# Kernel optimization log

Hardware: AMD Instinct MI355X
Metric: run time of the kernel (lower is better)

## Reference

```python
import jax, jax.numpy as jnp
import numpy as np

N = 100000; E = 3200000; B = 4096
F = 128; H = 128; T1 = 574; T2 = 152; MH = 128
BN_INV = float(1.0 / np.sqrt(1.0 + 1e-5))  # eval-mode BatchNorm1d, running_mean=0, running_var=1


def setup_inputs() -> dict:
    key = jax.random.key(0)
    ks = jax.random.split(key, 16)
    def w(k, shape):
        return (jax.random.normal(k, shape, jnp.float32) / np.sqrt(shape[0])).astype(jnp.float32)
    return {
        "feats": jax.random.normal(ks[0], (N, F), jnp.float32),
        "src": jax.random.randint(ks[1], (E,), 0, N, dtype=jnp.int32),
        "dst": jax.random.randint(ks[2], (E,), 0, N, dtype=jnp.int32),
        "graph_ids": jnp.sort(jax.random.randint(ks[3], (N,), 0, B, dtype=jnp.int32)),
        "W1": w(ks[4], (F, H)), "b1": jnp.zeros((H,), jnp.float32),
        "resW1": w(ks[5], (F, H)), "resb1": jnp.zeros((H,), jnp.float32),
        "W2": w(ks[6], (H, H)), "b2": jnp.zeros((H,), jnp.float32),
        "resW2": w(ks[7], (H, H)), "resb2": jnp.zeros((H,), jnp.float32),
        "aw_W": w(ks[8], (H, 1)), "aw_b": jnp.zeros((1,), jnp.float32),
        "orW1": w(ks[9], (2 * H, MH)), "orb1": jnp.zeros((MH,), jnp.float32),
        "org": jnp.ones((MH,), jnp.float32), "orbeta": jnp.zeros((MH,), jnp.float32),
        "orW2": w(ks[10], (MH, T1)), "orb2": jnp.zeros((T1,), jnp.float32),
        "scW1": w(ks[11], (2 * H + T1, MH)), "scb1": jnp.zeros((MH,), jnp.float32),
        "scg": jnp.ones((MH,), jnp.float32), "scbeta": jnp.zeros((MH,), jnp.float32),
        "scW2": w(ks[12], (MH, T2)), "scb2": jnp.zeros((T2,), jnp.float32),
    }


def _gcn_layer(feats, src, dst, W, b, resW, resb, out_norm, in_norm):
    # GraphConv with norm='both': D_out^{-1/2} on source, sum over edges, D_in^{-1/2} on dest.
    h = (feats * out_norm[:, None]) @ W                       # [N, H]
    agg = jax.ops.segment_sum(h[src], dst, num_segments=N)    # gather-compute-scatter
    out = jax.nn.relu(agg * in_norm[:, None] + b)             # activation inside GraphConv
    return out + jax.nn.relu(feats @ resW + resb)             # dgllife residual branch


def _mlp(x, Wa, ba, gam, bet, Wb, bb):
    # dgllife MLPPredictor: Dropout(0) -> Linear -> ReLU -> BatchNorm1d(eval) -> Linear
    z = jax.nn.relu(x @ Wa + ba)
    z = gam * (z * BN_INV) + bet
    return z @ Wb + bb


def _forward(feats, src, dst, graph_ids, W1, b1, resW1, resb1, W2, b2, resW2, resb2,
             aw_W, aw_b, orW1, orb1, org, orbeta, orW2, orb2,
             scW1, scb1, scg, scbeta, scW2, scb2):
    ones = jnp.ones((E,), jnp.float32)
    out_norm = jnp.clip(jax.ops.segment_sum(ones, src, num_segments=N), 1.0) ** -0.5
    in_norm = jnp.clip(jax.ops.segment_sum(ones, dst, num_segments=N), 1.0) ** -0.5
    h = _gcn_layer(feats, src, dst, W1, b1, resW1, resb1, out_norm, in_norm)
    h = _gcn_layer(h, src, dst, W2, b2, resW2, resb2, out_norm, in_norm)
    # WeightedSumAndMax readout
    aw = jax.nn.sigmoid(h @ aw_W + aw_b)                      # [N, 1] atom weights
    hsum = jax.ops.segment_sum(aw * h, graph_ids, num_segments=B)
    hmax = jax.ops.segment_max(h, graph_ids, num_segments=B)
    hmax = jnp.where(jnp.isfinite(hmax), hmax, 0.0)           # guard empty graphs
    g = jnp.concatenate([hsum, hmax], axis=1)                 # [B, 2H]
    or_logits = _mlp(g, orW1, orb1, org, orbeta, orW2, orb2)  # [B, T1]
    scent = _mlp(jnp.concatenate([g, or_logits], axis=1), scW1, scb1, scg, scbeta, scW2, scb2)
    return or_logits, scent


def reference(feats, src, dst, graph_ids, W1, b1, resW1, resb1, W2, b2, resW2, resb2,
              aw_W, aw_b, orW1, orb1, org, orbeta, orW2, orb2,
              scW1, scb1, scg, scbeta, scW2, scb2):
    return _forward(feats, src, dst, graph_ids, W1, b1, resW1, resb1, W2, b2, resW2, resb2,
                    aw_W, aw_b, orW1, orb1, org, orbeta, orW2, orb2,
                    scW1, scb1, scg, scbeta, scW2, scb2)
```

## Files before the change

### kernel.cpp

```cpp
#include <hip/hip_runtime.h>

#define NN 100000
#define EE 3200000
#define NGRAPH 4096
#define BN_INV_F 0.99999500003749981f
#define PAD 80
#define SHIFT 8
#define NBUCK 391
#define CHUNK 8192
#define NBLK 391
#define SCAN_N (2 * NBUCK * NBLK)
#define SCHUNK 2048
#define SBLKS ((SCAN_N + SCHUNK - 1) / SCHUNK)

typedef __attribute__((ext_vector_type(8))) short short8v;
typedef __attribute__((ext_vector_type(4))) float f32x4;

__device__ inline ushort f2bf(float f) {
  uint u = __builtin_bit_cast(uint, f);
  u += 0x7fff + ((u >> 16) & 1);
  return (ushort)(u >> 16);
}
__device__ inline float bf_lo(uint v) { return __builtin_bit_cast(float, v << 16); }
__device__ inline float bf_hi(uint v) { return __builtin_bit_cast(float, v & 0xffff0000u); }

__global__ __launch_bounds__(256) void count_ab(const int* __restrict__ src,
                                                const int* __restrict__ dst,
                                                int* __restrict__ cnt) {
  __shared__ int hd[NBUCK], hs[NBUCK];
  int t = threadIdx.x, blk = blockIdx.x;
  for (int i = t; i < NBUCK; i += 256) { hd[i] = 0; hs[i] = 0; }
  __syncthreads();
  int base = blk * CHUNK;
#pragma unroll 4
  for (int j = 0; j < 32; j++) {
    int e = base + j * 256 + t;
    if (e < EE) {
      atomicAdd(&hd[((unsigned)dst[e]) >> SHIFT], 1);
      atomicAdd(&hs[((unsigned)src[e]) >> SHIFT], 1);
    }
  }
  __syncthreads();
  for (int i = t; i < NBUCK; i += 256) {
    cnt[i * NBLK + blk] = hd[i];
    cnt[(NBUCK + i) * NBLK + blk] = hs[i];
  }
}

__global__ __launch_bounds__(256) void scan1(const int* __restrict__ cnt,
                                             int* __restrict__ partial) {
  __shared__ int red[256];
  int b = blockIdx.x, t = threadIdx.x;
  int s = 0;
  for (int j = 0; j < 8; j++) { int i = b * SCHUNK + j * 256 + t; if (i < SCAN_N) s += cnt[i]; }
  red[t] = s;
  __syncthreads();
  for (int off = 128; off > 0; off >>= 1) {
    if (t < off) red[t] += red[t + off];
    __syncthreads();
  }
  if (t == 0) partial[b] = red[0];
}

__global__ void scan2(int* __restrict__ partial) {
  if (threadIdx.x == 0) {
    int run = 0;
    for (int i = 0; i < SBLKS; i++) { int v = partial[i]; partial[i] = run; run += v; }
  }
}

__global__ __launch_bounds__(256) void scan3(int* __restrict__ cnt,
                                             const int* __restrict__ partial) {
  __shared__ int wsum[4];
  int b = blockIdx.x, t = threadIdx.x;
  int lane = t & 63, wid = t >> 6;
  int base = b * SCHUNK + t * 8;
  int v[8];
#pragma unroll
  for (int j = 0; j < 8; j++) { int i = base + j; v[j] = (i < SCAN_N) ? cnt[i] : 0; }
  int s = ((v[0] + v[1]) + (v[2] + v[3])) + ((v[4] + v[5]) + (v[6] + v[7]));
  int inc = s;
#pragma unroll
  for (int off = 1; off < 64; off <<= 1) {
    int u = __shfl_up(inc, off);
    if (lane >= off) inc += u;
  }
  if (lane == 63) wsum[wid] = inc;
  __syncthreads();
  int woff = 0;
  for (int w = 0; w < wid; w++) woff += wsum[w];
  int excl = partial[b] + woff + (inc - s);
#pragma unroll
  for (int j = 0; j < 8; j++) {
    int i = base + j;
    if (i < SCAN_N) cnt[i] = excl;
    excl += v[j];
  }
}

__global__ __launch_bounds__(256) void scatter_c(const int* __restrict__ src,
                                                 const int* __restrict__ dst,
                                                 const int* __restrict__ off,
                                                 int2* __restrict__ ebuf,
                                                 int* __restrict__ sbuf) {
  __shared__ int cd[NBUCK], cs[NBUCK];
  int t = threadIdx.x, blk = blockIdx.x;
  for (int i = t; i < NBUCK; i += 256) {
    cd[i] = off[i * NBLK + blk];
    cs[i] = off[(NBUCK + i) * NBLK + blk] - EE;
  }
  __syncthreads();
  int base = blk * CHUNK;
#pragma unroll 4
  for (int j = 0; j < 32; j++) {
    int e = base + j * 256 + t;
    if (e < EE) {
      int d = dst[e], s = src[e];
      int p = atomicAdd(&cd[((unsigned)d) >> SHIFT], 1);
      ebuf[p] = make_int2(d, s);
      int q = atomicAdd(&cs[((unsigned)s) >> SHIFT], 1);
      sbuf[q] = s;
    }
  }
}

__global__ __launch_bounds__(256) void pass_dd(const int* __restrict__ off,
                                               const int2* __restrict__ ebuf,
                                               const int* __restrict__ sbuf,
                                               int* __restrict__ csrp,
                                               int* __restrict__ icnt,
                                               float* __restrict__ inrm,
                                               float* __restrict__ onrm) {
  __shared__ int cur[256], cur2[256];
  int t = threadIdx.x, b = blockIdx.x;
  cur[t] = 0; cur2[t] = 0;
  __syncthreads();
  int node0 = b << SHIFT;
  int start = off[b * NBLK];
  int end = (b == NBUCK - 1) ? EE : off[(b + 1) * NBLK];
  for (int e = start + t; e < end; e += 256) {
    int2 p = ebuf[e];
    int pos = atomicAdd(&cur[p.x - node0], 1);
    if (pos < PAD) csrp[(size_t)p.x * PAD + pos] = p.y;
  }
  int s2 = off[(NBUCK + b) * NBLK] - EE;
  int e2 = (b == NBUCK - 1) ? EE : off[(NBUCK + b + 1) * NBLK] - EE;
  for (int e = s2 + t; e < e2; e += 256)
    atomicAdd(&cur2[sbuf[e] - node0], 1);
  __syncthreads();
  int node = node0 + t;
  if (node < NN) {
    int c = cur[t];
    icnt[node] = c;
    inrm[node] = rsqrtf(fmaxf((float)c, 1.f));
    onrm[node] = rsqrtf(fmaxf((float)cur2[t], 1.f));
  }
}

__global__ __launch_bounds__(256) void conv_all(
    const float* __restrict__ W1, const float* __restrict__ rW1,
    const float* __restrict__ W2, const float* __restrict__ rW2,
    const float* __restrict__ oW1, const float* __restrict__ oW2,
    const float* __restrict__ sW1, const float* __restrict__ sW2,
    ushort* __restrict__ Wt1, ushort* __restrict__ Wr1,
    ushort* __restrict__ Wt2, ushort* __restrict__ Wr2,
    ushort* __restrict__ Wm1, ushort* __restrict__ Wm2,
    ushort* __restrict__ Wm3, ushort* __restrict__ Wm4)
{
  int b = blockIdx.x;
  const float* W; ushort* O; int K, N, Kpad, c;
  if (b < 512) {
    int which = b >> 7; c = b & 127;
    K = 128; N = 128; Kpad = 128;
    W = which == 0 ? W1 : which == 1 ? rW1 : which == 2 ? W2 : rW2;
    O = which == 0 ? Wt1 : which == 1 ? Wr1 : which == 2 ? Wt2 : Wr2;
  } else if (b < 640)  { c = b - 512;  W = oW1; O = Wm1; K = 256; N = 128; Kpad = 256; }
  else if (b < 1216)   { c = b - 640;  W = oW2; O = Wm2; K = 128; N = 574; Kpad = 128; }
  else if (b < 1344)   { c = b - 1216; W = sW1; O = Wm3; K = 830; N = 128; Kpad = 832; }
  else                 { c = b - 1344; W = sW2; O = Wm4; K = 128; N = 152; Kpad = 128; }
  for (int k = threadIdx.x; k < Kpad; k += 256)
    O[(size_t)c * Kpad + k] = (c < N && k < K) ? f2bf(W[(size_t)k * N + c]) : (ushort)0;
}

__global__ __launch_bounds__(256) void conv_x(const float* __restrict__ X,
                                              ushort* __restrict__ Xb) {
  int i = blockIdx.x * 256 + threadIdx.x;
  float4 v = *(const float4*)&X[(size_t)i * 4];
  ushort o[4] = {f2bf(v.x), f2bf(v.y), f2bf(v.z), f2bf(v.w)};
  *(ushort4*)&Xb[(size_t)i * 4] = *(ushort4*)o;
}

__global__ __launch_bounds__(256) void gather_sc(const ushort* __restrict__ Xg,
                                                 const float* __restrict__ gscale,
                                                 const int* __restrict__ csrp,
                                                 const int* __restrict__ icnt,
                                                 ushort* __restrict__ Gbo) {
  int n  = blockIdx.x * 4 + (threadIdx.x >> 6);
  int c2 = threadIdx.x & 63;
  if (n >= NN) return;
  int cnt = icnt[n]; if (cnt > PAD) cnt = PAD;
  const int* row = csrp + (size_t)n * PAD;
  const uint* T32 = (const uint*)Xg;
  float a0 = 0.f, a1 = 0.f, b0 = 0.f, b1 = 0.f;
  float c0 = 0.f, c1 = 0.f, d0 = 0.f, d1 = 0.f;
  float e0 = 0.f, e1 = 0.f, f0 = 0.f, f1 = 0.f;
  float g0 = 0.f, g1 = 0.f, h0 = 0.f, h1 = 0.f;
  int j = 0;
  for (; j + 7 < cnt; j += 8) {
    int r0i = row[j],     r1i = row[j + 1], r2i = row[j + 2], r3i = row[j + 3];
    int r4i = row[j + 4], r5i = row[j + 5], r6i = row[j + 6], r7i = row[j + 7];
    float w0 = gscale[r0i], w1 = gscale[r1i], w2 = gscale[r2i], w3 = gscale[r3i];
    float w4 = gscale[r4i], w5 = gscale[r5i], w6 = gscale[r6i], w7 = gscale[r7i];
    uint v0 = T32[(size_t)r0i * 64 + c2];
    uint v1 = T32[(size_t)r1i * 64 + c2];
    uint v2 = T32[(size_t)r2i * 64 + c2];
    uint v3 = T32[(size_t)r3i * 64 + c2];
    uint v4 = T32[(size_t)r4i * 64 + c2];
    uint v5 = T32[(size_t)r5i * 64 + c2];
    uint v6 = T32[(size_t)r6i * 64 + c2];
    uint v7 = T32[(size_t)r7i * 64 + c2];
    a0 = fmaf(w0, bf_lo(v0), a0); a1 = fmaf(w0, bf_hi(v0), a1);
    b0 = fmaf(w1, bf_lo(v1), b0); b1 = fmaf(w1, bf_hi(v1), b1);
    c0 = fmaf(w2, bf_lo(v2), c0); c1 = fmaf(w2, bf_hi(v2), c1);
    d0 = fmaf(w3, bf_lo(v3), d0); d1 = fmaf(w3, bf_hi(v3), d1);
    e0 = fmaf(w4, bf_lo(v4), e0); e1 = fmaf(w4, bf_hi(v4), e1);
    f0 = fmaf(w5, bf_lo(v5), f0); f1 = fmaf(w5, bf_hi(v5), f1);
    g0 = fmaf(w6, bf_lo(v6), g0); g1 = fmaf(w6, bf_hi(v6), g1);
    h0 = fmaf(w7, bf_lo(v7), h0); h1 = fmaf(w7, bf_hi(v7), h1);
  }
  for (; j < cnt; j++) {
    int ri = row[j];
    float w = gscale[ri];
    uint v = T32[(size_t)ri * 64 + c2];
    a0 = fmaf(w, bf_lo(v), a0); a1 = fmaf(w, bf_hi(v), a1);
  }
  float s0 = ((a0 + b0) + (c0 + d0)) + ((e0 + f0) + (g0 + h0));
  float s1 = ((a1 + b1) + (c1 + d1)) + ((e1 + f1) + (g1 + h1));
  uint o = (uint)f2bf(s0) | ((uint)f2bf(s1) << 16);
  ((uint*)Gbo)[(size_t)n * 64 + c2] = o;
}

template<int MODE>
__global__ __launch_bounds__(256) void dual_gemm(
    const ushort* __restrict__ Gb, const ushort* __restrict__ Xr,
    const ushort* __restrict__ Wt, const ushort* __restrict__ Wr,
    const float* __restrict__ innorm,
    const float* __restrict__ bias, const float* __restrict__ resb,
    ushort* __restrict__ outb, float* __restrict__ outf,
    const float* __restrict__ awW, const float* __restrict__ awb,
    float* __restrict__ aw)
{
  int lane = threadIdx.x & 63;
  int wid  = threadIdx.x >> 6;
  int r0   = blockIdx.x * 64 + wid * 16;
  int cl = lane & 15, kh = lane >> 4;

  int arow = r0 + cl; if (arow > NN - 1) arow = NN - 1;
  short8v a1v[4], a2v[4];
#pragma unroll
  for (int kk = 0; kk < 4; kk++) {
    a1v[kk] = *(const short8v*)(Gb + (size_t)arow * 128 + kk * 32 + kh * 8);
    a2v[kk] = *(const short8v*)(Xr + (size_t)arow * 128 + kk * 32 + kh * 8);
  }

  f32x4 acc1[8], acc2[8];
#pragma unroll
  for (int i = 0; i < 8; i++) { acc1[i] = (f32x4){0.f,0.f,0.f,0.f}; acc2[i] = acc1[i]; }
#pragma unroll
  for (int ct = 0; ct < 8; ct++) {
#pragma unroll
    for (int kk = 0; kk < 4; kk++) {
      short8v bt = *(const short8v*)(Wt + (size_t)(ct * 16 + cl) * 128 + kk * 32 + kh * 8);
      short8v br = *(const short8v*)(Wr + (size_t)(ct * 16 + cl) * 128 + kk * 32 + kh * 8);
      acc1[ct] = __builtin_amdgcn_mfma_f32_16x16x32_bf16(a1v[kk], bt, acc1[ct], 0, 0, 0);
      acc2[ct] = __builtin_amdgcn_mfma_f32_16x16x32_bf16(a2v[kk], br, acc2[ct], 0, 0, 0);
    }
  }

#pragma unroll
  for (int r = 0; r < 4; r++) {
    int row = r0 + kh * 4 + r;
    if (row >= NN) continue;
    float inr = innorm[row];
    float pr = 0.f;
#pragma unroll
    for (int ct = 0; ct < 8; ct++) {
      int col = ct * 16 + cl;
      float g  = acc1[ct][r] * inr + bias[col];
      float rs = acc2[ct][r] + resb[col];
      float v = fmaxf(g, 0.f) + fmaxf(rs, 0.f);
      if (MODE == 1) outb[(size_t)row * 128 + col] = f2bf(v);
      else { outf[(size_t)row * 128 + col] = v; pr += v * awW[col]; }
    }
    if (MODE == 2) {
#pragma unroll
      for (int off = 1; off < 16; off <<= 1) pr += __shfl_xor(pr, off);
      if (cl == 0) aw[row] = 1.f / (1.f + expf(-(pr + awb[0])));
    }
  }
}

__global__ void readout_kernel(const float* __restrict__ h,
                               const float* __restrict__ aw,
                               const int* __restrict__ gid,
                               ushort* __restrict__ xc)
{
  int gg = blockIdx.x;
  int c  = threadIdx.x;
  int lo = 0, hi = NN;
  while (lo < hi) { int mid = (lo + hi) >> 1; if (gid[mid] < gg) lo = mid + 1; else hi = mid; }
  int start = lo;
  hi = NN;
  while (lo < hi) { int mid = (lo + hi) >> 1; if (gid[mid] < gg + 1) lo = mid + 1; else hi = mid; }
  int end = lo;
  float s = 0.f, m = 0.f;
  for (int n = start; n < end; n++) {
    float v = h[(size_t)n * 128 + c];
    s += aw[n] * v;
    m = fmaxf(m, v);
  }
  xc[(size_t)gg * 256 + c]       = f2bf(s);
  xc[(size_t)gg * 256 + 128 + c] = f2bf(m);
}

__global__ __launch_bounds__(256) void head2_mfma(
    const ushort* __restrict__ xc,
    const ushort* __restrict__ Wm1, const float* __restrict__ orb1,
    const float* __restrict__ org, const float* __restrict__ orbeta,
    const ushort* __restrict__ Wm2, const float* __restrict__ orb2,
    const ushort* __restrict__ Wm3, const float* __restrict__ scb1,
    const float* __restrict__ scg, const float* __restrict__ scbeta,
    const ushort* __restrict__ Wm4, const float* __restrict__ scb2,
    float* __restrict__ out_or, float* __restrict__ out_sc)
{
  __shared__ ushort zl[16][136];
  __shared__ ushort lg[16][584];
  int lane = threadIdx.x & 63;
  int wid  = threadIdx.x >> 6;
  int r0   = blockIdx.x * 16;
  int cl = lane & 15, kh = lane >> 4;
  int arow = r0 + cl;

  {
    short8v a[8];
#pragma unroll
    for (int kk = 0; kk < 8; kk++)
      a[kk] = *(const short8v*)(xc + (size_t)arow * 256 + kk * 32 + kh * 8);
    for (int ct = wid; ct < 8; ct += 4) {
      f32x4 acc = (f32x4){0.f, 0.f, 0.f, 0.f};
#pragma unroll
      for (int kk = 0; kk < 8; kk++) {
        short8v b = *(const short8v*)(Wm1 + (size_t)(ct * 16 + cl) * 256 + kk * 32 + kh * 8);
        acc = __builtin_amdgcn_mfma_f32_16x16x32_bf16(a[kk], b, acc, 0, 0, 0);
      }
      int col = ct * 16 + cl;
      float bz = orb1[col], gm = org[col], bt = orbeta[col];
#pragma unroll
      for (int r = 0; r < 4; r++) {
        float v = acc[r] + bz;
        zl[kh * 4 + r][col] = f2bf(gm * (fmaxf(v, 0.f) * BN_INV_F) + bt);
      }
    }
  }
  __syncthreads();

  {
    short8v za[4];
#pragma unroll
    for (int kk = 0; kk < 4; kk++)
      za[kk] = *(const short8v*)&zl[cl][kk * 32 + kh * 8];
    for (int ct = wid; ct < 36; ct += 4) {
      f32x4 acc = (f32x4){0.f, 0.f, 0.f, 0.f};
#pragma unroll
      for (int kk = 0; kk < 4; kk++) {
        short8v b = *(const short8v*)(Wm2 + (size_t)(ct * 16 + cl) * 128 + kk * 32 + kh * 8);
        acc = __builtin_amdgcn_mfma_f32_16x16x32_bf16(za[kk], b, acc, 0, 0, 0);
      }
      int col = ct * 16 + cl;
      if (col < 574) {
        float bz = orb2[col];
#pragma unroll
        for (int r = 0; r < 4; r++) {
          int row = r0 + kh * 4 + r;
          float v = acc[r] + bz;
          out_or[(size_t)row * 574 + col] = v;
          lg[kh * 4 + r][col] = f2bf(v);
        }
      } else {
#pragma unroll
        for (int r = 0; r < 4; r++) lg[kh * 4 + r][col] = 0;
      }
    }
  }
  __syncthreads();

  {
    short8v a[26];
#pragma unroll
    for (int kk = 0; kk < 8; kk++)
      a[kk] = *(const short8v*)(xc + (size_t)arow * 256 + kk * 32 + kh * 8);
#pragma unroll
    for (int kk = 8; kk < 26; kk++)
      a[kk] = *(const short8v*)&lg[cl][(kk - 8) * 32 + kh * 8];
    for (int ct = wid; ct < 8; ct += 4) {
      f32x4 acc = (f32x4){0.f, 0.f, 0.f, 0.f};
#pragma unroll
      for (int kk = 0; kk < 26; kk++) {
        short8v b = *(const short8v*)(Wm3 + (size_t)(ct * 16 + cl) * 832 + kk * 32 + kh * 8);
        acc = __builtin_amdgcn_mfma_f32_16x16x32_bf16(a[kk], b, acc, 0, 0, 0);
      }
      int col = ct * 16 + cl;
      float bz = scb1[col], gm = scg[col], bt = scbeta[col];
#pragma unroll
      for (int r = 0; r < 4; r++) {
        float v = acc[r] + bz;
        zl[kh * 4 + r][col] = f2bf(gm * (fmaxf(v, 0.f) * BN_INV_F) + bt);
      }
    }
  }
  __syncthreads();

  {
    short8v za[4];
#pragma unroll
    for (int kk = 0; kk < 4; kk++)
      za[kk] = *(const short8v*)&zl[cl][kk * 32 + kh * 8];
    for (int ct = wid; ct < 10; ct += 4) {
      f32x4 acc = (f32x4){0.f, 0.f, 0.f, 0.f};
#pragma unroll
      for (int kk = 0; kk < 4; kk++) {
        short8v b = *(const short8v*)(Wm4 + (size_t)(ct * 16 + cl) * 128 + kk * 32 + kh * 8);
        acc = __builtin_amdgcn_mfma_f32_16x16x32_bf16(za[kk], b, acc, 0, 0, 0);
      }
      int col = ct * 16 + cl;
      if (col < 152) {
        float bz = scb2[col];
#pragma unroll
        for (int r = 0; r < 4; r++) {
          int row = r0 + kh * 4 + r;
          out_sc[(size_t)row * 152 + col] = acc[r] + bz;
        }
      }
    }
  }
}

extern "C" void kernel_launch(void* const* d_in, const int* in_sizes, int n_in,
                              void* d_out, int out_size, void* d_ws, size_t ws_size,
                              hipStream_t stream) {
  const float* feats  = (const float*)d_in[0];
  const int*   src    = (const int*)d_in[1];
  const int*   dst    = (const int*)d_in[2];
  const int*   gid    = (const int*)d_in[3];
  const float* W1     = (const float*)d_in[4];
  const float* b1     = (const float*)d_in[5];
  const float* resW1  = (const float*)d_in[6];
  const float* resb1  = (const float*)d_in[7];
  const float* W2     = (const float*)d_in[8];
  const float* b2     = (const float*)d_in[9];
  const float* resW2  = (const float*)d_in[10];
  const float* resb2  = (const float*)d_in[11];
  const float* awW    = (const float*)d_in[12];
  const float* awb    = (const float*)d_in[13];
  const float* orW1   = (const float*)d_in[14];
  const float* orb1   = (const float*)d_in[15];
  const float* org    = (const float*)d_in[16];
  const float* orbeta = (const float*)d_in[17];
  const float* orW2   = (const float*)d_in[18];
  const float* orb2   = (const float*)d_in[19];
  const float* scW1   = (const float*)d_in[20];
  const float* scb1   = (const float*)d_in[21];
  const float* scg    = (const float*)d_in[22];
  const float* scbeta = (const float*)d_in[23];
  const float* scW2   = (const float*)d_in[24];
  const float* scb2   = (const float*)d_in[25];

  char* base = (char*)d_ws;
  ushort* Xb = (ushort*)base;
  ushort* Lb = Xb + (size_t)NN * 128;
  ushort* Gb = Lb + (size_t)NN * 128;
  float*  Hf = (float*)(Gb + (size_t)NN * 128);
  int2*   ebuf = (int2*)Hf;
  int*    sbuf = (int*)(Hf + (size_t)NN * 64);
  ushort* xc  = (ushort*)(Hf + (size_t)NN * 128);
  ushort* Wt1 = xc + (size_t)NGRAPH * 256;
  ushort* Wr1 = Wt1 + 128 * 128;
  ushort* Wt2 = Wr1 + 128 * 128;
  ushort* Wr2 = Wt2 + 128 * 128;
  ushort* Wm1 = Wr2 + 128 * 128;
  ushort* Wm2 = Wm1 + 128 * 256;
  ushort* Wm3 = Wm2 + 576 * 128;
  ushort* Wm4 = Wm3 + 128 * 832;
  float* onrm = (float*)(Wm4 + 160 * 128);
  float* inrm = onrm + NN;
  float* aw   = inrm + NN;
  int* icnt    = (int*)(aw + NN);
  int* cnt     = icnt + NN;
  int* partial = cnt + SCAN_N;
  int* csrp    = partial + SBLKS;

  float* out_or = (float*)d_out;
  float* out_sc = out_or + (size_t)NGRAPH * 574;

  count_ab<<<NBLK, 256, 0, stream>>>(src, dst, cnt);
  scan1<<<SBLKS, 256, 0, stream>>>(cnt, partial);
  scan2<<<1, 64, 0, stream>>>(partial);
  scan3<<<SBLKS, 256, 0, stream>>>(cnt, partial);
  scatter_c<<<NBLK, 256, 0, stream>>>(src, dst, cnt, ebuf, sbuf);
  pass_dd<<<NBUCK, 256, 0, stream>>>(cnt, ebuf, sbuf, csrp, icnt, inrm, onrm);
  conv_all<<<1504, 256, 0, stream>>>(W1, resW1, W2, resW2, orW1, orW2, scW1, scW2,
                                     Wt1, Wr1, Wt2, Wr2, Wm1, Wm2, Wm3, Wm4);
  conv_x<<<12500, 256, 0, stream>>>(feats, Xb);

  int ggrid = (NN + 3) / 4;
  int dgrid = (NN + 63) / 64;
  gather_sc<<<ggrid, 256, 0, stream>>>(Xb, onrm, csrp, icnt, Gb);
  dual_gemm<1><<<dgrid, 256, 0, stream>>>(Gb, Xb, Wt1, Wr1, inrm, b1, resb1,
                                          Lb, nullptr, nullptr, nullptr, nullptr);
  gather_sc<<<ggrid, 256, 0, stream>>>(Lb, onrm, csrp, icnt, Gb);
  dual_gemm<2><<<dgrid, 256, 0, stream>>>(Gb, Lb, Wt2, Wr2, inrm, b2, resb2,
                                          nullptr, Hf, awW, awb, aw);
  readout_kernel<<<NGRAPH, 128, 0, stream>>>(Hf, aw, gid, xc);
  head2_mfma<<<NGRAPH / 16, 256, 0, stream>>>(xc, Wm1, orb1, org, orbeta, Wm2, orb2,
                                              Wm3, scb1, scg, scbeta, Wm4, scb2,
                                              out_or, out_sc);
}
```

Measured before the change: 581.9 us.

## Transform features before gathering and fuse fp32-to-bf16 conversion into first GEMM

Result: faster. 536.5 us (-7.8%).

```diff
diff --git a/kernel.cpp b/kernel.cpp
--- a/kernel.cpp
+++ b/kernel.cpp
@@ -21,6 +21,7 @@
   u += 0x7fff + ((u >> 16) & 1);
   return (ushort)(u >> 16);
 }
+__device__ inline float bf2f(ushort v) { return __builtin_bit_cast(float, (uint)v << 16); }
 __device__ inline float bf_lo(uint v) { return __builtin_bit_cast(float, v << 16); }
 __device__ inline float bf_hi(uint v) { return __builtin_bit_cast(float, v & 0xffff0000u); }
 
@@ -182,25 +183,108 @@
     O[(size_t)c * Kpad + k] = (c < N && k < K) ? f2bf(W[(size_t)k * N + c]) : (ushort)0;
 }
 
-__global__ __launch_bounds__(256) void conv_x(const float* __restrict__ X,
-                                              ushort* __restrict__ Xb) {
-  int i = blockIdx.x * 256 + threadIdx.x;
-  float4 v = *(const float4*)&X[(size_t)i * 4];
-  ushort o[4] = {f2bf(v.x), f2bf(v.y), f2bf(v.z), f2bf(v.w)};
-  *(ushort4*)&Xb[(size_t)i * 4] = *(ushort4*)o;
-}
-
-__global__ __launch_bounds__(256) void gather_sc(const ushort* __restrict__ Xg,
-                                                 const float* __restrict__ gscale,
-                                                 const int* __restrict__ csrp,
-                                                 const int* __restrict__ icnt,
-                                                 ushort* __restrict__ Gbo) {
+template<int MODE>
+__global__ __launch_bounds__(256) void gemm_mfma(
+    const ushort* __restrict__ Xin, const float* __restrict__ Xf,
+    ushort* __restrict__ Xbout,
+    const ushort* __restrict__ Wt,
+    const float* __restrict__ rowscale,
+    const ushort* __restrict__ Gb, const float* __restrict__ innorm,
+    const float* __restrict__ bias, const float* __restrict__ resb,
+    ushort* __restrict__ outb, float* __restrict__ outf,
+    const float* __restrict__ awW, const float* __restrict__ awb,
+    float* __restrict__ aw)
+{
+  int lane = threadIdx.x & 63;
+  int wid  = threadIdx.x >> 6;
+  int r0   = blockIdx.x * 128 + wid * 32;
+  int cl = lane & 15, kh = lane >> 4;
+
+  short8v a[2][4];
+#pragma unroll
+  for (int g = 0; g < 2; g++) {
+    int row  = r0 + g * 16 + cl;
+    int rowc = row < NN ? row : NN - 1;
+    if (MODE == 3) {
+#pragma unroll
+      for (int kk = 0; kk < 4; kk++) {
+        const float* p = Xf + (size_t)rowc * 128 + kk * 32 + kh * 8;
+        float4 v0 = *(const float4*)p;
+        float4 v1 = *(const float4*)(p + 4);
+        short8v t;
+        t[0] = (short)f2bf(v0.x); t[1] = (short)f2bf(v0.y);
+        t[2] = (short)f2bf(v0.z); t[3] = (short)f2bf(v0.w);
+        t[4] = (short)f2bf(v1.x); t[5] = (short)f2bf(v1.y);
+        t[6] = (short)f2bf(v1.z); t[7] = (short)f2bf(v1.w);
+        a[g][kk] = t;
+        if (row < NN)
+          *(short8v*)(Xbout + (size_t)row * 128 + kk * 32 + kh * 8) = t;
+      }
+    } else {
+#pragma unroll
+      for (int kk = 0; kk < 4; kk++)
+        a[g][kk] = *(const short8v*)(Xin + (size_t)rowc * 128 + kk * 32 + kh * 8);
+    }
+  }
+
+  f32x4 acc[2][8];
+#pragma unroll
+  for (int g = 0; g < 2; g++)
+#pragma unroll
+    for (int t = 0; t < 8; t++) acc[g][t] = (f32x4){0.f, 0.f, 0.f, 0.f};
+
+#pragma unroll
+  for (int ct = 0; ct < 8; ct++) {
+#pragma unroll
+    for (int kk = 0; kk < 4; kk++) {
+      short8v b = *(const short8v*)(Wt + (size_t)(ct * 16 + cl) * 128 + kk * 32 + kh * 8);
+      acc[0][ct] = __builtin_amdgcn_mfma_f32_16x16x32_bf16(a[0][kk], b, acc[0][ct], 0, 0, 0);
+      acc[1][ct] = __builtin_amdgcn_mfma_f32_16x16x32_bf16(a[1][kk], b, acc[1][ct], 0, 0, 0);
+    }
+  }
+
+#pragma unroll
+  for (int g = 0; g < 2; g++)
+#pragma unroll
+  for (int r = 0; r < 4; r++) {
+    int row = r0 + g * 16 + kh * 4 + r;
+    if (row >= NN) continue;
+    if (MODE == 0 || MODE == 3) {
+      float s = rowscale[row];
+#pragma unroll
+      for (int ct = 0; ct < 8; ct++)
+        outb[(size_t)row * 128 + ct * 16 + cl] = f2bf(acc[g][ct][r] * s);
+    } else {
+      float inr = innorm[row];
+      float pr = 0.f;
+#pragma unroll
+      for (int ct = 0; ct < 8; ct++) {
+        int col = ct * 16 + cl;
+        float gg  = bf2f(Gb[(size_t)row * 128 + col]) * inr + bias[col];
+        float res = acc[g][ct][r] + resb[col];
+        float v = fmaxf(gg, 0.f) + fmaxf(res, 0.f);
+        if (MODE == 1) outb[(size_t)row * 128 + col] = f2bf(v);
+        else { outf[(size_t)row * 128 + col] = v; pr += v * awW[col]; }
+      }
+      if (MODE == 2) {
+#pragma unroll
+        for (int off = 1; off < 16; off <<= 1) pr += __shfl_xor(pr, off);
+        if (cl == 0) aw[row] = 1.f / (1.f + expf(-(pr + awb[0])));
+      }
+    }
+  }
+}
+
+__global__ __launch_bounds__(256) void gather_bf16(const ushort* __restrict__ Tb,
+                                                   const int* __restrict__ csrp,
+                                                   const int* __restrict__ icnt,
+                                                   ushort* __restrict__ Gbo) {
   int n  = blockIdx.x * 4 + (threadIdx.x >> 6);
   int c2 = threadIdx.x & 63;
   if (n >= NN) return;
   int cnt = icnt[n]; if (cnt > PAD) cnt = PAD;
   const int* row = csrp + (size_t)n * PAD;
-  const uint* T32 = (const uint*)Xg;
+  const uint* T32 = (const uint*)Tb;
   float a0 = 0.f, a1 = 0.f, b0 = 0.f, b1 = 0.f;
   float c0 = 0.f, c1 = 0.f, d0 = 0.f, d1 = 0.f;
   float e0 = 0.f, e1 = 0.f, f0 = 0.f, f1 = 0.f;
@@ -209,8 +293,6 @@
   for (; j + 7 < cnt; j += 8) {
     int r0i = row[j],     r1i = row[j + 1], r2i = row[j + 2], r3i = row[j + 3];
     int r4i = row[j + 4], r5i = row[j + 5], r6i = row[j + 6], r7i = row[j + 7];
-    float w0 = gscale[r0i], w1 = gscale[r1i], w2 = gscale[r2i], w3 = gscale[r3i];
-    float w4 = gscale[r4i], w5 = gscale[r5i], w6 = gscale[r6i], w7 = gscale[r7i];
     uint v0 = T32[(size_t)r0i * 64 + c2];
     uint v1 = T32[(size_t)r1i * 64 + c2];
     uint v2 = T32[(size_t)r2i * 64 + c2];
@@ -219,85 +301,23 @@
     uint v5 = T32[(size_t)r5i * 64 + c2];
     uint v6 = T32[(size_t)r6i * 64 + c2];
     uint v7 = T32[(size_t)r7i * 64 + c2];
-    a0 = fmaf(w0, bf_lo(v0), a0); a1 = fmaf(w0, bf_hi(v0), a1);
-    b0 = fmaf(w1, bf_lo(v1), b0); b1 = fmaf(w1, bf_hi(v1), b1);
-    c0 = fmaf(w2, bf_lo(v2), c0); c1 = fmaf(w2, bf_hi(v2), c1);
-    d0 = fmaf(w3, bf_lo(v3), d0); d1 = fmaf(w3, bf_hi(v3), d1);
-    e0 = fmaf(w4, bf_lo(v4), e0); e1 = fmaf(w4, bf_hi(v4), e1);
-    f0 = fmaf(w5, bf_lo(v5), f0); f1 = fmaf(w5, bf_hi(v5), f1);
-    g0 = fmaf(w6, bf_lo(v6), g0); g1 = fmaf(w6, bf_hi(v6), g1);
-    h0 = fmaf(w7, bf_lo(v7), h0); h1 = fmaf(w7, bf_hi(v7), h1);
+    a0 += bf_lo(v0); a1 += bf_hi(v0);
+    b0 += bf_lo(v1); b1 += bf_hi(v1);
+    c0 += bf_lo(v2); c1 += bf_hi(v2);
+    d0 += bf_lo(v3); d1 += bf_hi(v3);
+    e0 += bf_lo(v4); e1 += bf_hi(v4);
+    f0 += bf_lo(v5); f1 += bf_hi(v5);
+    g0 += bf_lo(v6); g1 += bf_hi(v6);
+    h0 += bf_lo(v7); h1 += bf_hi(v7);
   }
   for (; j < cnt; j++) {
-    int ri = row[j];
-    float w = gscale[ri];
-    uint v = T32[(size_t)ri * 64 + c2];
-    a0 = fmaf(w, bf_lo(v), a0); a1 = fmaf(w, bf_hi(v), a1);
+    uint v = T32[(size_t)row[j] * 64 + c2];
+    a0 += bf_lo(v); a1 += bf_hi(v);
   }
   float s0 = ((a0 + b0) + (c0 + d0)) + ((e0 + f0) + (g0 + h0));
   float s1 = ((a1 + b1) + (c1 + d1)) + ((e1 + f1) + (g1 + h1));
   uint o = (uint)f2bf(s0) | ((uint)f2bf(s1) << 16);
   ((uint*)Gbo)[(size_t)n * 64 + c2] = o;
-}
-
-template<int MODE>
-__global__ __launch_bounds__(256) void dual_gemm(
-    const ushort* __restrict__ Gb, const ushort* __restrict__ Xr,
-    const ushort* __restrict__ Wt, const ushort* __restrict__ Wr,
-    const float* __restrict__ innorm,
-    const float* __restrict__ bias, const float* __restrict__ resb,
-    ushort* __restrict__ outb, float* __restrict__ outf,
-    const float* __restrict__ awW, const float* __restrict__ awb,
-    float* __restrict__ aw)
-{
-  int lane = threadIdx.x & 63;
-  int wid  = threadIdx.x >> 6;
-  int r0   = blockIdx.x * 64 + wid * 16;
-  int cl = lane & 15, kh = lane >> 4;
-
-  int arow = r0 + cl; if (arow > NN - 1) arow = NN - 1;
-  short8v a1v[4], a2v[4];
-#pragma unroll
-  for (int kk = 0; kk < 4; kk++) {
-    a1v[kk] = *(const short8v*)(Gb + (size_t)arow * 128 + kk * 32 + kh * 8);
-    a2v[kk] = *(const short8v*)(Xr + (size_t)arow * 128 + kk * 32 + kh * 8);
-  }
-
-  f32x4 acc1[8], acc2[8];
-#pragma unroll
-  for (int i = 0; i < 8; i++) { acc1[i] = (f32x4){0.f,0.f,0.f,0.f}; acc2[i] = acc1[i]; }
-#pragma unroll
-  for (int ct = 0; ct < 8; ct++) {
-#pragma unroll
-    for (int kk = 0; kk < 4; kk++) {
-      short8v bt = *(const short8v*)(Wt + (size_t)(ct * 16 + cl) * 128 + kk * 32 + kh * 8);
-      short8v br = *(const short8v*)(Wr + (size_t)(ct * 16 + cl) * 128 + kk * 32 + kh * 8);
-      acc1[ct] = __builtin_amdgcn_mfma_f32_16x16x32_bf16(a1v[kk], bt, acc1[ct], 0, 0, 0);
-      acc2[ct] = __builtin_amdgcn_mfma_f32_16x16x32_bf16(a2v[kk], br, acc2[ct], 0, 0, 0);
-    }
-  }
-
-#pragma unroll
-  for (int r = 0; r < 4; r++) {
-    int row = r0 + kh * 4 + r;
-    if (row >= NN) continue;
-    float inr = innorm[row];
-    float pr = 0.f;
-#pragma unroll
-    for (int ct = 0; ct < 8; ct++) {
-      int col = ct * 16 + cl;
-      float g  = acc1[ct][r] * inr + bias[col];
-      float rs = acc2[ct][r] + resb[col];
-      float v = fmaxf(g, 0.f) + fmaxf(rs, 0.f);
-      if (MODE == 1) outb[(size_t)row * 128 + col] = f2bf(v);
-      else { outf[(size_t)row * 128 + col] = v; pr += v * awW[col]; }
-    }
-    if (MODE == 2) {
-#pragma unroll
-      for (int off = 1; off < 16; off <<= 1) pr += __shfl_xor(pr, off);
-      if (cl == 0) aw[row] = 1.f / (1.f + expf(-(pr + awb[0])));
-    }
-  }
 }
 
 __global__ void readout_kernel(const float* __restrict__ h,
@@ -477,7 +497,8 @@
 
   char* base = (char*)d_ws;
   ushort* Xb = (ushort*)base;
-  ushort* Lb = Xb + (size_t)NN * 128;
+  ushort* Tb = Xb + (size_t)NN * 128;
+  ushort* Lb = Tb + (size_t)NN * 128;
   ushort* Gb = Lb + (size_t)NN * 128;
   float*  Hf = (float*)(Gb + (size_t)NN * 128);
   int2*   ebuf = (int2*)Hf;
@@ -510,16 +531,23 @@
   pass_dd<<<NBUCK, 256, 0, stream>>>(cnt, ebuf, sbuf, csrp, icnt, inrm, onrm);
   conv_all<<<1504, 256, 0, stream>>>(W1, resW1, W2, resW2, orW1, orW2, scW1, scW2,
                                      Wt1, Wr1, Wt2, Wr2, Wm1, Wm2, Wm3, Wm4);
-  conv_x<<<12500, 256, 0, stream>>>(feats, Xb);
-
+
+  int gemm_grid = (NN + 127) / 128;
   int ggrid = (NN + 3) / 4;
-  int dgrid = (NN + 63) / 64;
-  gather_sc<<<ggrid, 256, 0, stream>>>(Xb, onrm, csrp, icnt, Gb);
-  dual_gemm<1><<<dgrid, 256, 0, stream>>>(Gb, Xb, Wt1, Wr1, inrm, b1, resb1,
-                                          Lb, nullptr, nullptr, nullptr, nullptr);
-  gather_sc<<<ggrid, 256, 0, stream>>>(Lb, onrm, csrp, icnt, Gb);
-  dual_gemm<2><<<dgrid, 256, 0, stream>>>(Gb, Lb, Wt2, Wr2, inrm, b2, resb2,
-                                          nullptr, Hf, awW, awb, aw);
+  gemm_mfma<3><<<gemm_grid, 256, 0, stream>>>(nullptr, feats, Xb, Wt1, onrm,
+                                              nullptr, nullptr, nullptr, nullptr,
+                                              Tb, nullptr, nullptr, nullptr, nullptr);
+  gather_bf16<<<ggrid, 256, 0, stream>>>(Tb, csrp, icnt, Gb);
+  gemm_mfma<1><<<gemm_grid, 256, 0, stream>>>(Xb, nullptr, nullptr, Wr1, nullptr,
+                                              Gb, inrm, b1, resb1,
+                                              Lb, nullptr, nullptr, nullptr, nullptr);
+  gemm_mfma<0><<<gemm_grid, 256, 0, stream>>>(Lb, nullptr, nullptr, Wt2, onrm,
+                                              nullptr, nullptr, nullptr, nullptr,
+                                              Tb, nullptr, nullptr, nullptr, nullptr);
+  gather_bf16<<<ggrid, 256, 0, stream>>>(Tb, csrp, icnt, Gb);
+  gemm_mfma<2><<<gemm_grid, 256, 0, stream>>>(Lb, nullptr, nullptr, Wr2, nullptr,
+                                              Gb, inrm, b2, resb2,
+                                              nullptr, Hf, awW, awb, aw);
   readout_kernel<<<NGRAPH, 128, 0, stream>>>(Hf, aw, gid, xc);
   head2_mfma<<<NGRAPH / 16, 256, 0, stream>>>(xc, Wm1, orb1, org, orbeta, Wm2, orb2,
                                               Wm3, scb1, scg, scbeta, Wm4, scb2,
```
